# Kernel tuning notes

Hardware: AMD Instinct MI355X
Metric: run time of the kernel (lower is better)

## Reference

```python
import jax, jax.numpy as jnp
import numpy as np

LORA_SCALING = 16.0 / 8.0  # lora_alpha / lora_r


def setup_inputs() -> dict:
    key = jax.random.key(0)
    k_x, k_m, k_wm, k_bm, k_wa, k_wb = jax.random.split(key, 6)
    B, S, D_in, D_out, R = 4, 2048, 4096, 4096, 8
    x = jax.random.normal(k_x, (B, S, D_in), dtype=jnp.float32)
    im_mask = jax.random.randint(k_m, (B, S), 0, 2) > 0  # bool token mask
    # Linear weights stored torch-style: [out, in]
    W_main = jax.random.normal(k_wm, (D_out, D_in), dtype=jnp.float32) * (1.0 / np.sqrt(D_in))
    b_main = jax.random.normal(k_bm, (D_out,), dtype=jnp.float32) * 0.01
    W_A = jax.random.normal(k_wa, (R, D_in), dtype=jnp.float32) * (1.0 / np.sqrt(D_in))
    W_B = jax.random.normal(k_wb, (D_out, R), dtype=jnp.float32) * (1.0 / np.sqrt(R))
    return {"x": x, "im_mask": im_mask, "W_main": W_main, "b_main": b_main, "W_A": W_A, "W_B": W_B}


def reference(x, im_mask, W_main, b_main, W_A, W_B):
    # Main dense path: res = x @ W_main.T + b
    res = jnp.einsum('bsd,od->bso', x, W_main) + b_main
    # LoRA path applied only at masked tokens (dropout disabled / eval):
    # res[im_mask] += (x[im_mask] @ W_A.T) @ W_B.T * scaling
    # Static-shape equivalent: compute everywhere, mask the add.
    lora = jnp.einsum('bsr,or->bso', jnp.einsum('bsd,rd->bsr', x, W_A), W_B)
    return res + jnp.where(im_mask[..., None], lora * LORA_SCALING, jnp.zeros((), x.dtype))
```

## Files before the change

### kernel.cpp

```cpp
#include <hip/hip_runtime.h>

typedef unsigned short u16;
typedef unsigned int   u32;
typedef unsigned long long u64;
typedef __bf16 bf16x8 __attribute__((ext_vector_type(8)));
typedef float  f32x4  __attribute__((ext_vector_type(4)));

#define AS1 __attribute__((address_space(1)))
#define AS3 __attribute__((address_space(3)))

#define M_TOK 8192
#define K_DIM 4096
#define N_DIM 4096
#define BK    32
#define NKT   (K_DIM / BK)

static __device__ __forceinline__ u16 f2bf(float f) {
  u32 u = __builtin_bit_cast(u32, f);
  return (u16)((u + (0x7FFFu + ((u >> 16) & 1u))) >> 16);
}

static __device__ __forceinline__ void gld_lds16(const void* g, void* l) {
  __builtin_amdgcn_global_load_lds((AS1 u32*)(u64)g, (AS3 u32*)(u32)(u64)l, 16, 0, 0);
}

__global__ __launch_bounds__(256) void k_prep(const float* __restrict__ x,
                                              const float* __restrict__ WA,
                                              const float* __restrict__ W,
                                              u16* __restrict__ xb,
                                              float* __restrict__ mid,
                                              u16* __restrict__ Wb) {
  const int t = threadIdx.x;
  if (blockIdx.x >= M_TOK) {
    const int cb = blockIdx.x - M_TOK;
    const float4* W4 = (const float4*)W;
    ushort4* Wb4 = (ushort4*)Wb;
    const int n4 = (N_DIM * K_DIM) / 4;
    int i = cb * 256 + t;
    for (; i < n4; i += 2048 * 256) {
      float4 v = W4[i];
      ushort4 o;
      o.x = f2bf(v.x); o.y = f2bf(v.y); o.z = f2bf(v.z); o.w = f2bf(v.w);
      Wb4[i] = o;
    }
    return;
  }
  const int m = blockIdx.x;
  const float4* xr = (const float4*)(x + (size_t)m * K_DIM);
  ushort4* xbr = (ushort4*)(xb + (size_t)m * K_DIM);
  float a[8] = {0.f,0.f,0.f,0.f,0.f,0.f,0.f,0.f};
  #pragma unroll
  for (int i = 0; i < 4; ++i) {
    const int k4 = t + i * 256;
    float4 v = xr[k4];
    ushort4 o;
    o.x = f2bf(v.x); o.y = f2bf(v.y); o.z = f2bf(v.z); o.w = f2bf(v.w);
    xbr[k4] = o;
    #pragma unroll
    for (int r = 0; r < 8; ++r) {
      float4 wv = ((const float4*)(WA + (size_t)r * K_DIM))[k4];
      a[r] += v.x * wv.x + v.y * wv.y + v.z * wv.z + v.w * wv.w;
    }
  }
  #pragma unroll
  for (int r = 0; r < 8; ++r) {
    #pragma unroll
    for (int off = 32; off > 0; off >>= 1)
      a[r] += __shfl_down(a[r], off);
  }
  __shared__ float red[4][8];
  const int w = t >> 6, l = t & 63;
  if (l == 0) {
    #pragma unroll
    for (int r = 0; r < 8; ++r) red[w][r] = a[r];
  }
  __syncthreads();
  if (t < 8)
    mid[(size_t)m * 8 + t] = 2.0f * (red[0][t] + red[1][t] + red[2][t] + red[3][t]);
}

__global__ __launch_bounds__(512, 2) void k_gemm(
    const u16* __restrict__ A, const u16* __restrict__ B,
    const float* __restrict__ bias, const int* __restrict__ mask,
    const float* __restrict__ mid, const float* __restrict__ WBw,
    float* __restrict__ out) {
  __shared__ u16 smem[4][2][256][BK];

  const int t = threadIdx.x;
  const int wid = t >> 6, l = t & 63;
  const int wr = wid >> 2, wc = wid & 3;
  const int fr = l & 15, fq = l >> 4;

  const int bid = blockIdx.x;
  const int swz = (bid & 7) * 64 + (bid >> 3);
  const int bm = swz >> 4, bn = swz & 15;

  const char* Ag = (const char*)(A + (size_t)bm * 256 * K_DIM);
  const char* Bg = (const char*)(B + (size_t)bn * 256 * K_DIM);
  const size_t rowb = (size_t)K_DIM * 2;

  const int srow = t >> 2;
  const int schk = (((t & 3) ^ ((t >> 3) & 3)) * 16);
  const char* bA0 = Ag + (size_t)srow * rowb + schk;
  const char* bA1 = Ag + (size_t)(128 + srow) * rowb + schk;
  const char* bB0 = Bg + (size_t)srow * rowb + schk;
  const char* bB1 = Bg + (size_t)(128 + srow) * rowb + schk;
  char* lbase = (char*)&smem[0][0][0][0] + wid * 1024;

  f32x4 acc[8][4];
  #pragma unroll
  for (int m = 0; m < 8; ++m)
    #pragma unroll
    for (int n = 0; n < 4; ++n)
      acc[m][n] = (f32x4){0.f, 0.f, 0.f, 0.f};

  #pragma unroll
  for (int pk = 0; pk < 3; ++pk) {
    gld_lds16(bA0 + pk * 64, lbase + pk * 32768);
    gld_lds16(bA1 + pk * 64, lbase + pk * 32768 + 8192);
    gld_lds16(bB0 + pk * 64, lbase + pk * 32768 + 16384);
    gld_lds16(bB1 + pk * 64, lbase + pk * 32768 + 24576);
  }
  asm volatile("s_waitcnt vmcnt(8)");
  __builtin_amdgcn_s_barrier();

  const int csw = (fq ^ ((fr >> 1) & 3)) * 8;

  const char* gA0 = bA0 + 192;
  const char* gA1 = bA1 + 192;
  const char* gB0 = bB0 + 192;
  const char* gB1 = bB1 + 192;

  #define K_TILE(BUFC, NB, DOSTAGE, GOFF, WAIT) do {                         \
    const u16* Ab_ = &smem[BUFC][0][wr * 128 + fr][csw];                     \
    const u16* Bb_ = &smem[BUFC][1][wc * 64 + fr][csw];                      \
    bf16x8 af_[8], bf_[4];                                                   \
    _Pragma("unroll")                                                        \
    for (int m = 0; m < 8; ++m) af_[m] = *(const bf16x8*)(Ab_ + m * 16 * BK);\
    _Pragma("unroll")                                                        \
    for (int n = 0; n < 4; ++n) bf_[n] = *(const bf16x8*)(Bb_ + n * 16 * BK);\
    if (DOSTAGE) {                                                           \
      gld_lds16(gA0 + (GOFF), lbase + (NB) * 32768);                         \
      gld_lds16(gA1 + (GOFF), lbase + (NB) * 32768 + 8192);                  \
      gld_lds16(gB0 + (GOFF), lbase + (NB) * 32768 + 16384);                 \
      gld_lds16(gB1 + (GOFF), lbase + (NB) * 32768 + 24576);                 \
    }                                                                        \
    __builtin_amdgcn_s_setprio(1);                                           \
    _Pragma("unroll")                                                        \
    for (int m = 0; m < 8; ++m)                                              \
      _Pragma("unroll")                                                      \
      for (int n = 0; n < 4; ++n)                                            \
        acc[m][n] = __builtin_amdgcn_mfma_f32_16x16x32_bf16(                 \
            af_[m], bf_[n], acc[m][n], 0, 0, 0);                             \
    __builtin_amdgcn_s_setprio(0);                                           \
    WAIT;                                                                    \
    __builtin_amdgcn_s_barrier();                                            \
  } while (0)

  #define VM8 asm volatile("s_waitcnt vmcnt(8)")
  #define VM4 asm volatile("s_waitcnt vmcnt(4)")
  #define VM0 asm volatile("s_waitcnt vmcnt(0)")

  for (int ktb = 0; ktb < NKT - 4; ktb += 4) {
    K_TILE(0, 3, true, 0,   VM8);
    K_TILE(1, 0, true, 64,  VM8);
    K_TILE(2, 1, true, 128, VM8);
    K_TILE(3, 2, true, 192, VM8);
    gA0 += 256; gA1 += 256; gB0 += 256; gB1 += 256;
  }
  K_TILE(0, 3, true,  0, VM8);
  K_TILE(1, 0, false, 0, VM4);
  K_TILE(2, 1, false, 0, VM0);
  K_TILE(3, 2, false, 0, ((void)0));

  #undef K_TILE
  #undef VM8
  #undef VM4
  #undef VM0

  const int gn0 = bn * 256 + wc * 64;
  const size_t gm0 = (size_t)bm * 256 + wr * 128;
  float wbv[4][8]; float bv[4];
  #pragma unroll
  for (int n = 0; n < 4; ++n) {
    const int gn = gn0 + n * 16 + fr;
    bv[n] = bias[gn];
    const float4 w0 = ((const float4*)(WBw + (size_t)gn * 8))[0];
    const float4 w1 = ((const float4*)(WBw + (size_t)gn * 8))[1];
    wbv[n][0] = w0.x; wbv[n][1] = w0.y; wbv[n][2] = w0.z; wbv[n][3] = w0.w;
    wbv[n][4] = w1.x; wbv[n][5] = w1.y; wbv[n][6] = w1.z; wbv[n][7] = w1.w;
  }
  #pragma unroll
  for (int m = 0; m < 8; ++m) {
    #pragma unroll
    for (int j = 0; j < 4; ++j) {
      const size_t gm = gm0 + m * 16 + fq * 4 + j;
      const int msk = mask[gm];
      const float4 m0 = ((const float4*)(mid + gm * 8))[0];
      const float4 m1 = ((const float4*)(mid + gm * 8))[1];
      float* orow = out + gm * (size_t)N_DIM;
      #pragma unroll
      for (int n = 0; n < 4; ++n) {
        const float lora =
            m0.x * wbv[n][0] + m0.y * wbv[n][1] + m0.z * wbv[n][2] + m0.w * wbv[n][3] +
            m1.x * wbv[n][4] + m1.y * wbv[n][5] + m1.z * wbv[n][6] + m1.w * wbv[n][7];
        orow[gn0 + n * 16 + fr] = acc[m][n][j] + bv[n] + (msk ? lora : 0.0f);
      }
    }
  }
}

extern "C" void kernel_launch(void* const* d_in, const int* in_sizes, int n_in,
                              void* d_out, int out_size, void* d_ws, size_t ws_size,
                              hipStream_t stream) {
  (void)in_sizes; (void)n_in; (void)out_size; (void)ws_size;
  const float* x     = (const float*)d_in[0];
  const int*   mask  = (const int*)d_in[1];
  const float* Wm    = (const float*)d_in[2];
  const float* bmain = (const float*)d_in[3];
  const float* WA    = (const float*)d_in[4];
  const float* WB    = (const float*)d_in[5];
  float* out = (float*)d_out;

  u16* xb  = (u16*)d_ws;
  u16* wb  = xb + (size_t)M_TOK * K_DIM;
  float* mid = (float*)(wb + (size_t)N_DIM * K_DIM);

  k_prep<<<M_TOK + 2048, 256, 0, stream>>>(x, WA, Wm, xb, mid, wb);
  dim3 grid((M_TOK / 256) * (N_DIM / 256));
  k_gemm<<<grid, 512, 0, stream>>>(xb, wb, bmain, mask, mid, WB, out);
}
```

Before: 325.9 us.

## Double-buffer MFMA operand fragments in registers to overlap LDS reads with compute

The K loop now keeps two register sets of A/B fragments. Each tile runs its MFMAs on fragments read during the previous tile, while it issues the LDS reads for the next buffer. The global-to-LDS staging wait is tightened from vmcnt(8) to vmcnt(4) so the next LDS buffer is ready before the early fragment read. The aim is to hide LDS read latency behind matrix math. The cost is about 48 extra VGPRs, which could lower occupancy, and less slack in the global-load pipeline.

```diff
diff --git a/kernel.cpp b/kernel.cpp
--- a/kernel.cpp
+++ b/kernel.cpp
@@ -121,7 +121,7 @@
     gld_lds16(bB0 + pk * 64, lbase + pk * 32768 + 16384);
     gld_lds16(bB1 + pk * 64, lbase + pk * 32768 + 24576);
   }
-  asm volatile("s_waitcnt vmcnt(8)");
+  asm volatile("s_waitcnt vmcnt(4)" ::: "memory");
   __builtin_amdgcn_s_barrier();
 
   const int csw = (fq ^ ((fr >> 1) & 3)) * 8;
@@ -131,52 +131,67 @@
   const char* gB0 = bB0 + 192;
   const char* gB1 = bB1 + 192;
 
-  #define K_TILE(BUFC, NB, DOSTAGE, GOFF, WAIT) do {                         \
-    const u16* Ab_ = &smem[BUFC][0][wr * 128 + fr][csw];                     \
-    const u16* Bb_ = &smem[BUFC][1][wc * 64 + fr][csw];                      \
-    bf16x8 af_[8], bf_[4];                                                   \
-    _Pragma("unroll")                                                        \
-    for (int m = 0; m < 8; ++m) af_[m] = *(const bf16x8*)(Ab_ + m * 16 * BK);\
-    _Pragma("unroll")                                                        \
-    for (int n = 0; n < 4; ++n) bf_[n] = *(const bf16x8*)(Bb_ + n * 16 * BK);\
-    if (DOSTAGE) {                                                           \
-      gld_lds16(gA0 + (GOFF), lbase + (NB) * 32768);                         \
-      gld_lds16(gA1 + (GOFF), lbase + (NB) * 32768 + 8192);                  \
-      gld_lds16(gB0 + (GOFF), lbase + (NB) * 32768 + 16384);                 \
-      gld_lds16(gB1 + (GOFF), lbase + (NB) * 32768 + 24576);                 \
-    }                                                                        \
-    __builtin_amdgcn_s_setprio(1);                                           \
-    _Pragma("unroll")                                                        \
-    for (int m = 0; m < 8; ++m)                                              \
-      _Pragma("unroll")                                                      \
-      for (int n = 0; n < 4; ++n)                                            \
-        acc[m][n] = __builtin_amdgcn_mfma_f32_16x16x32_bf16(                 \
-            af_[m], bf_[n], acc[m][n], 0, 0, 0);                             \
-    __builtin_amdgcn_s_setprio(0);                                           \
-    WAIT;                                                                    \
-    __builtin_amdgcn_s_barrier();                                            \
+  bf16x8 afA[8], bfA[4], afB[8], bfB[4];
+
+  {
+    const u16* Ap_ = &smem[0][0][wr * 128 + fr][csw];
+    const u16* Bp_ = &smem[0][1][wc * 64 + fr][csw];
+    #pragma unroll
+    for (int m = 0; m < 8; ++m) afA[m] = *(const bf16x8*)(Ap_ + m * 16 * BK);
+    #pragma unroll
+    for (int n = 0; n < 4; ++n) bfA[n] = *(const bf16x8*)(Bp_ + n * 16 * BK);
+  }
+
+  #define K_TILE(PBUF, CURA, CURB, ALTA, ALTB, DOSTAGE, NB, GOFF, WAIT, DOPF) \
+  do {                                                                        \
+    if (DOSTAGE) {                                                            \
+      gld_lds16(gA0 + (GOFF), lbase + (NB) * 32768);                          \
+      gld_lds16(gA1 + (GOFF), lbase + (NB) * 32768 + 8192);                   \
+      gld_lds16(gB0 + (GOFF), lbase + (NB) * 32768 + 16384);                  \
+      gld_lds16(gB1 + (GOFF), lbase + (NB) * 32768 + 24576);                  \
+    }                                                                         \
+    WAIT;                                                                     \
+    if (DOPF) {                                                               \
+      const u16* Ap_ = &smem[PBUF][0][wr * 128 + fr][csw];                    \
+      const u16* Bp_ = &smem[PBUF][1][wc * 64 + fr][csw];                     \
+      _Pragma("unroll")                                                       \
+      for (int m = 0; m < 8; ++m)                                             \
+        ALTA[m] = *(const bf16x8*)(Ap_ + m * 16 * BK);                        \
+      _Pragma("unroll")                                                       \
+      for (int n = 0; n < 4; ++n)                                             \
+        ALTB[n] = *(const bf16x8*)(Bp_ + n * 16 * BK);                        \
+    }                                                                         \
+    __builtin_amdgcn_s_setprio(1);                                            \
+    _Pragma("unroll")                                                         \
+    for (int m = 0; m < 8; ++m)                                               \
+      _Pragma("unroll")                                                       \
+      for (int n = 0; n < 4; ++n)                                             \
+        acc[m][n] = __builtin_amdgcn_mfma_f32_16x16x32_bf16(                  \
+            CURA[m], CURB[n], acc[m][n], 0, 0, 0);                            \
+    __builtin_amdgcn_s_setprio(0);                                            \
+    __builtin_amdgcn_s_barrier();                                             \
   } while (0)
 
-  #define VM8 asm volatile("s_waitcnt vmcnt(8)")
-  #define VM4 asm volatile("s_waitcnt vmcnt(4)")
-  #define VM0 asm volatile("s_waitcnt vmcnt(0)")
+  #define VMW4 asm volatile("s_waitcnt vmcnt(4)" ::: "memory")
+  #define VMW0 asm volatile("s_waitcnt vmcnt(0)" ::: "memory")
+  #define NOW  ((void)0)
 
   for (int ktb = 0; ktb < NKT - 4; ktb += 4) {
-    K_TILE(0, 3, true, 0,   VM8);
-    K_TILE(1, 0, true, 64,  VM8);
-    K_TILE(2, 1, true, 128, VM8);
-    K_TILE(3, 2, true, 192, VM8);
+    K_TILE(1, afA, bfA, afB, bfB, true, 3, 0,   VMW4, true);
+    K_TILE(2, afB, bfB, afA, bfA, true, 0, 64,  VMW4, true);
+    K_TILE(3, afA, bfA, afB, bfB, true, 1, 128, VMW4, true);
+    K_TILE(0, afB, bfB, afA, bfA, true, 2, 192, VMW4, true);
     gA0 += 256; gA1 += 256; gB0 += 256; gB1 += 256;
   }
-  K_TILE(0, 3, true,  0, VM8);
-  K_TILE(1, 0, false, 0, VM4);
-  K_TILE(2, 1, false, 0, VM0);
-  K_TILE(3, 2, false, 0, ((void)0));
+  K_TILE(1, afA, bfA, afB, bfB, true,  3, 0, VMW4, true);
+  K_TILE(2, afB, bfB, afA, bfA, false, 0, 0, VMW0, true);
+  K_TILE(3, afA, bfA, afB, bfB, false, 0, 0, NOW,  true);
+  K_TILE(0, afB, bfB, afA, bfA, false, 0, 0, NOW,  false);
 
   #undef K_TILE
-  #undef VM8
-  #undef VM4
-  #undef VM0
+  #undef VMW4
+  #undef VMW0
+  #undef NOW
 
   const int gn0 = bn * 256 + wc * 64;
   const size_t gm0 = (size_t)bm * 256 + wr * 128;
```

New measurement: 362.3 us. 1.11x slower.

## Software-pipeline LDS fragment reads for next tile under current MFMAs

Applied to the files above, without the earlier changes.

Register fragments for the next K tile are now prefetched from LDS while the current tile's MFMAs run, splitting the MFMA block into two halves with the reads interleaved between them. The global-to-LDS wait depth is tightened (vmcnt 8 to 4) so the next buffer is ready one stage earlier. The aim is to hide LDS read latency behind matrix math. In exchange, the effective prefetch distance of global loads shrinks and register pressure rises, which could lower occupancy or expose memory latency.

```diff
diff --git a/kernel.cpp b/kernel.cpp
--- a/kernel.cpp
+++ b/kernel.cpp
@@ -121,7 +121,7 @@
     gld_lds16(bB0 + pk * 64, lbase + pk * 32768 + 16384);
     gld_lds16(bB1 + pk * 64, lbase + pk * 32768 + 24576);
   }
-  asm volatile("s_waitcnt vmcnt(8)");
+  asm volatile("s_waitcnt vmcnt(4)" ::: "memory");
   __builtin_amdgcn_s_barrier();
 
   const int csw = (fq ^ ((fr >> 1) & 3)) * 8;
@@ -131,52 +131,82 @@
   const char* gB0 = bB0 + 192;
   const char* gB1 = bB1 + 192;
 
-  #define K_TILE(BUFC, NB, DOSTAGE, GOFF, WAIT) do {                         \
-    const u16* Ab_ = &smem[BUFC][0][wr * 128 + fr][csw];                     \
-    const u16* Bb_ = &smem[BUFC][1][wc * 64 + fr][csw];                      \
-    bf16x8 af_[8], bf_[4];                                                   \
-    _Pragma("unroll")                                                        \
-    for (int m = 0; m < 8; ++m) af_[m] = *(const bf16x8*)(Ab_ + m * 16 * BK);\
-    _Pragma("unroll")                                                        \
-    for (int n = 0; n < 4; ++n) bf_[n] = *(const bf16x8*)(Bb_ + n * 16 * BK);\
+  bf16x8 af[8], bf[4];
+
+  {
+    const u16* Ap_ = &smem[0][0][wr * 128 + fr][csw];
+    const u16* Bp_ = &smem[0][1][wc * 64 + fr][csw];
+    #pragma unroll
+    for (int m = 0; m < 8; ++m) af[m] = *(const bf16x8*)(Ap_ + m * 16 * BK);
+    #pragma unroll
+    for (int n = 0; n < 4; ++n) bf[n] = *(const bf16x8*)(Bp_ + n * 16 * BK);
+  }
+
+  #define K_TILE(RBUF, SB, DOSTAGE, DOREAD, GOFF, WAIT) do {                 \
     if (DOSTAGE) {                                                           \
-      gld_lds16(gA0 + (GOFF), lbase + (NB) * 32768);                         \
-      gld_lds16(gA1 + (GOFF), lbase + (NB) * 32768 + 8192);                  \
-      gld_lds16(gB0 + (GOFF), lbase + (NB) * 32768 + 16384);                 \
-      gld_lds16(gB1 + (GOFF), lbase + (NB) * 32768 + 24576);                 \
+      gld_lds16(gA0 + (GOFF), lbase + (SB) * 32768);                         \
+      gld_lds16(gA1 + (GOFF), lbase + (SB) * 32768 + 8192);                  \
+      gld_lds16(gB0 + (GOFF), lbase + (SB) * 32768 + 16384);                 \
+      gld_lds16(gB1 + (GOFF), lbase + (SB) * 32768 + 24576);                 \
     }                                                                        \
     __builtin_amdgcn_s_setprio(1);                                           \
     _Pragma("unroll")                                                        \
-    for (int m = 0; m < 8; ++m)                                              \
+    for (int m = 0; m < 4; ++m)                                              \
       _Pragma("unroll")                                                      \
       for (int n = 0; n < 4; ++n)                                            \
         acc[m][n] = __builtin_amdgcn_mfma_f32_16x16x32_bf16(                 \
-            af_[m], bf_[n], acc[m][n], 0, 0, 0);                             \
+            af[m], bf[n], acc[m][n], 0, 0, 0);                               \
     __builtin_amdgcn_s_setprio(0);                                           \
+    if (DOREAD) {                                                            \
+      const u16* Ap_ = &smem[RBUF][0][wr * 128 + fr][csw];                   \
+      _Pragma("unroll")                                                      \
+      for (int m = 0; m < 4; ++m)                                            \
+        af[m] = *(const bf16x8*)(Ap_ + m * 16 * BK);                         \
+    }                                                                        \
+    __builtin_amdgcn_sched_barrier(0);                                       \
+    __builtin_amdgcn_s_setprio(1);                                           \
+    _Pragma("unroll")                                                        \
+    for (int m = 4; m < 8; ++m)                                              \
+      _Pragma("unroll")                                                      \
+      for (int n = 0; n < 4; ++n)                                            \
+        acc[m][n] = __builtin_amdgcn_mfma_f32_16x16x32_bf16(                 \
+            af[m], bf[n], acc[m][n], 0, 0, 0);                               \
+    __builtin_amdgcn_s_setprio(0);                                           \
+    if (DOREAD) {                                                            \
+      const u16* Ap_ = &smem[RBUF][0][wr * 128 + fr][csw];                   \
+      const u16* Bp_ = &smem[RBUF][1][wc * 64 + fr][csw];                    \
+      _Pragma("unroll")                                                      \
+      for (int m = 4; m < 8; ++m)                                            \
+        af[m] = *(const bf16x8*)(Ap_ + m * 16 * BK);                         \
+      _Pragma("unroll")                                                      \
+      for (int n = 0; n < 4; ++n)                                            \
+        bf[n] = *(const bf16x8*)(Bp_ + n * 16 * BK);                         \
+    }                                                                        \
+    __builtin_amdgcn_sched_barrier(0);                                       \
     WAIT;                                                                    \
     __builtin_amdgcn_s_barrier();                                            \
   } while (0)
 
-  #define VM8 asm volatile("s_waitcnt vmcnt(8)")
-  #define VM4 asm volatile("s_waitcnt vmcnt(4)")
-  #define VM0 asm volatile("s_waitcnt vmcnt(0)")
+  #define VM4 asm volatile("s_waitcnt vmcnt(4)" ::: "memory")
+  #define VM0 asm volatile("s_waitcnt vmcnt(0)" ::: "memory")
+  #define NOW ((void)0)
 
   for (int ktb = 0; ktb < NKT - 4; ktb += 4) {
-    K_TILE(0, 3, true, 0,   VM8);
-    K_TILE(1, 0, true, 64,  VM8);
-    K_TILE(2, 1, true, 128, VM8);
-    K_TILE(3, 2, true, 192, VM8);
+    K_TILE(1, 3, true, true, 0,   VM4);
+    K_TILE(2, 0, true, true, 64,  VM4);
+    K_TILE(3, 1, true, true, 128, VM4);
+    K_TILE(0, 2, true, true, 192, VM4);
     gA0 += 256; gA1 += 256; gB0 += 256; gB1 += 256;
   }
-  K_TILE(0, 3, true,  0, VM8);
-  K_TILE(1, 0, false, 0, VM4);
-  K_TILE(2, 1, false, 0, VM0);
-  K_TILE(3, 2, false, 0, ((void)0));
+  K_TILE(1, 3, true,  true,  0, VM4);
+  K_TILE(2, 0, false, true,  0, VM0);
+  K_TILE(3, 0, false, true,  0, NOW);
+  K_TILE(0, 0, false, false, 0, NOW);
 
   #undef K_TILE
-  #undef VM8
   #undef VM4
   #undef VM0
+  #undef NOW
 
   const int gn0 = bn * 256 + wc * 64;
   const size_t gm0 = (size_t)bm * 256 + wr * 128;
```

Result: no change. 326.5 us, median of 2 (+0.2%).
